# Kernel optimization log

Hardware: AMD Instinct MI355X
Metric: run time of the kernel (lower is better)

The kernel has to match this reference:

```python
import jax, jax.numpy as jnp
import numpy as np

D = 1024      # hidden_size
H = 16        # num_heads
HD = D // H   # head_dim = 64
FF = 4096     # intermediate_size
DEPTH = 2
S = 2048      # packed sequence length
NSEG = 4     # number of image segments
EPS = 1e-6


def setup_inputs() -> dict:
    key = jax.random.key(0)
    ks = jax.random.split(key, 8)
    hidden_states = jax.random.normal(ks[0], (S, D), jnp.float32)
    cu_seqlens = jnp.arange(NSEG + 1, dtype=jnp.int32) * (S // NSEG)
    # rotary embedding like RiceRotaryEmbedding(head_dim//2): freqs of dim HD//4
    # per spatial axis, h/w concatenated -> HD//2, then duplicated -> HD
    inv_freq = 1.0 / (10000.0 ** (jnp.arange(0, HD // 2, 2, dtype=jnp.float32) / (HD // 2)))
    pos = jnp.arange(S, dtype=jnp.float32)
    freqs = jnp.outer(pos, inv_freq)                       # [S, HD//4]
    emb = jnp.concatenate([freqs] * 4, axis=-1)            # [S, HD]
    cos, sin = jnp.cos(emb), jnp.sin(emb)

    def w(k, shape, fan):
        return jax.random.normal(k, shape, jnp.float32) / np.sqrt(fan)

    return {
        "hidden_states": hidden_states,
        "cu_seqlens": cu_seqlens,
        "cos": cos,
        "sin": sin,
        "ln1_g": jnp.ones((DEPTH, D), jnp.float32),
        "ln1_b": jnp.zeros((DEPTH, D), jnp.float32),
        "qkv_w": w(ks[1], (DEPTH, D, 3 * D), D),
        "qkv_b": jnp.zeros((DEPTH, 3 * D), jnp.float32),
        "proj_w": w(ks[2], (DEPTH, D, D), D),
        "proj_b": jnp.zeros((DEPTH, D), jnp.float32),
        "ln2_g": jnp.ones((DEPTH, D), jnp.float32),
        "ln2_b": jnp.zeros((DEPTH, D), jnp.float32),
        "fc1_w": w(ks[3], (DEPTH, D, FF), D),
        "fc1_b": jnp.zeros((DEPTH, FF), jnp.float32),
        "fc2_w": w(ks[4], (DEPTH, FF, D), FF),
        "fc2_b": jnp.zeros((DEPTH, D), jnp.float32),
    }


def _ln(x, g, b):
    m = jnp.mean(x, axis=-1, keepdims=True)
    v = jnp.mean(jnp.square(x - m), axis=-1, keepdims=True)
    return (x - m) / jnp.sqrt(v + EPS) * g + b


def _rotate_half(x):
    x1, x2 = jnp.split(x, 2, axis=-1)
    return jnp.concatenate([-x2, x1], axis=-1)


def reference(hidden_states, cu_seqlens, cos, sin,
              ln1_g, ln1_b, qkv_w, qkv_b, proj_w, proj_b,
              ln2_g, ln2_b, fc1_w, fc1_b, fc2_w, fc2_b):
    S_, D_ = hidden_states.shape
    # segment id per token from cu_seqlens -> block-diagonal additive mask
    seg = jnp.searchsorted(cu_seqlens[1:], jnp.arange(S_, dtype=jnp.int32), side="right")
    neg = jnp.finfo(jnp.float32).min
    bias = jnp.where(seg[:, None] == seg[None, :], 0.0, neg)   # [S, S]
    cos_e = cos[:, None, :]  # broadcast over heads, [S,1,HD]
    sin_e = sin[:, None, :]
    scale = 1.0 / np.sqrt(HD)

    x = hidden_states
    for i in range(DEPTH):
        # --- attention ---
        h = _ln(x, ln1_g[i], ln1_b[i])
        qkv = h @ qkv_w[i] + qkv_b[i]                           # [S, 3D]
        q, k, v = [t.reshape(S_, H, HD) for t in jnp.split(qkv, 3, axis=-1)]
        q = q * cos_e + _rotate_half(q) * sin_e
        k = k * cos_e + _rotate_half(k) * sin_e
        scores = jnp.einsum("shd,thd->hst", q, k) * scale + bias  # [H,S,S]
        w_ = jax.nn.softmax(scores.astype(jnp.float32), axis=-1)
        ao = jnp.einsum("hst,thd->shd", w_, v).reshape(S_, D_)
        x = x + ao @ proj_w[i] + proj_b[i]
        # --- mlp ---
        h2 = _ln(x, ln2_g[i], ln2_b[i])
        x = x + jax.nn.gelu(h2 @ fc1_w[i] + fc1_b[i], approximate=False) @ fc2_w[i] + fc2_b[i]
    return x
```

## Files before the change

### kernel.cpp

```cpp
#include <hip/hip_runtime.h>
#include <hip/hip_bf16.h>
#include <math.h>

#define Dm 1024
#define Hn 16
#define HDm 64
#define FFm 4096
#define Sn 2048
#define SEG 512
#define EPSV 1e-6f

typedef __attribute__((ext_vector_type(4))) float f32x4;
typedef __attribute__((ext_vector_type(8))) short s16x8;
typedef __attribute__((ext_vector_type(4))) short s16x4;

__device__ inline short f2bf(float f) {
  __hip_bfloat16 h = __float2bfloat16(f);
  short s;
  __builtin_memcpy(&s, &h, 2);
  return s;
}
__device__ inline float bf2f(short s) {
  unsigned u = ((unsigned)(unsigned short)s) << 16;
  float f;
  __builtin_memcpy(&f, &u, 4);
  return f;
}

__device__ inline float wred_sum(float v) {
#pragma unroll
  for (int m = 32; m > 0; m >>= 1) v += __shfl_xor(v, m, 64);
  return v;
}

__device__ inline void gld16(const short* g, short* lds_base) {
  __builtin_amdgcn_global_load_lds(
      (const __attribute__((address_space(1))) void*)g,
      (__attribute__((address_space(3))) void*)lds_base, 16, 0, 0);
}

__global__ __launch_bounds__(256) void ln_kernel(const float* __restrict__ x,
                                                 const float* __restrict__ g,
                                                 const float* __restrict__ b,
                                                 short* __restrict__ out) {
  const int row = blockIdx.x;
  const int tid = threadIdx.x;
  f32x4 v = *reinterpret_cast<const f32x4*>(x + (size_t)row * Dm + tid * 4);
  float s1 = v.x + v.y + v.z + v.w;
  float s2 = v.x * v.x + v.y * v.y + v.z * v.z + v.w * v.w;
  s1 = wred_sum(s1);
  s2 = wred_sum(s2);
  __shared__ float t1[4], t2[4];
  if ((tid & 63) == 0) { t1[tid >> 6] = s1; t2[tid >> 6] = s2; }
  __syncthreads();
  s1 = t1[0] + t1[1] + t1[2] + t1[3];
  s2 = t2[0] + t2[1] + t2[2] + t2[3];
  const float mean = s1 * (1.0f / Dm);
  const float var = s2 * (1.0f / Dm) - mean * mean;
  const float rstd = rsqrtf(var + EPSV);
  f32x4 gv = *reinterpret_cast<const f32x4*>(g + tid * 4);
  f32x4 bv = *reinterpret_cast<const f32x4*>(b + tid * 4);
  s16x4 o;
#pragma unroll
  for (int j = 0; j < 4; ++j)
    o[j] = f2bf((v[j] - mean) * rstd * gv[j] + bv[j]);
  *reinterpret_cast<s16x4*>(out + (size_t)row * Dm + tid * 4) = o;
}

template <int SPLIT>
__global__ __launch_bounds__(256) void redln_bf(const short* __restrict__ pb,
                                                const float* __restrict__ bias,
                                                const float* __restrict__ res,
                                                const float* __restrict__ g,
                                                const float* __restrict__ b,
                                                float* __restrict__ xout,
                                                short* __restrict__ h) {
  const int row = blockIdx.x;
  const int tid = threadIdx.x;
  const size_t idx = (size_t)row * Dm + tid * 4;
  f32x4 o = *reinterpret_cast<const f32x4*>(res + idx);
  o += *reinterpret_cast<const f32x4*>(bias + tid * 4);
#pragma unroll
  for (int s = 0; s < SPLIT; ++s) {
    s16x4 v = *reinterpret_cast<const s16x4*>(pb + (size_t)s * Sn * Dm + idx);
#pragma unroll
    for (int j = 0; j < 4; ++j) o[j] += bf2f(v[j]);
  }
  *reinterpret_cast<f32x4*>(xout + idx) = o;
  float s1 = o.x + o.y + o.z + o.w;
  float s2 = o.x * o.x + o.y * o.y + o.z * o.z + o.w * o.w;
  s1 = wred_sum(s1);
  s2 = wred_sum(s2);
  __shared__ float t1[4], t2[4];
  if ((tid & 63) == 0) { t1[tid >> 6] = s1; t2[tid >> 6] = s2; }
  __syncthreads();
  s1 = t1[0] + t1[1] + t1[2] + t1[3];
  s2 = t2[0] + t2[1] + t2[2] + t2[3];
  const float mean = s1 * (1.0f / Dm);
  const float var = s2 * (1.0f / Dm) - mean * mean;
  const float rstd = rsqrtf(var + EPSV);
  f32x4 gv = *reinterpret_cast<const f32x4*>(g + tid * 4);
  f32x4 bv = *reinterpret_cast<const f32x4*>(b + tid * 4);
  s16x4 ho;
#pragma unroll
  for (int j = 0; j < 4; ++j)
    ho[j] = f2bf((o[j] - mean) * rstd * gv[j] + bv[j]);
  *reinterpret_cast<s16x4*>(h + idx) = ho;
}

template <int SPLIT>
__global__ __launch_bounds__(256) void fcred_bf(const short* __restrict__ pb,
                                                const float* __restrict__ bias,
                                                const float* __restrict__ res,
                                                float* __restrict__ out) {
  const size_t i = ((size_t)blockIdx.x * 256 + threadIdx.x) * 4;
  f32x4 o = *reinterpret_cast<const f32x4*>(res + i);
  o += *reinterpret_cast<const f32x4*>(bias + (i & (Dm - 1)));
#pragma unroll
  for (int s = 0; s < SPLIT; ++s) {
    s16x4 v = *reinterpret_cast<const s16x4*>(pb + (size_t)s * Sn * Dm + i);
#pragma unroll
    for (int j = 0; j < 4; ++j) o[j] += bf2f(v[j]);
  }
  *reinterpret_cast<f32x4*>(out + i) = o;
}

__global__ __launch_bounds__(256) void wt_kernel(const float* __restrict__ W,
                                                 short* __restrict__ Wt,
                                                 int K, int N, int ldw) {
  __shared__ float t[32][33];
  const int n0 = blockIdx.x * 32, k0 = blockIdx.y * 32;
  const int tx = threadIdx.x & 31, ty = threadIdx.x >> 5;
#pragma unroll
  for (int r = 0; r < 32; r += 8)
    t[r + ty][tx] = W[(size_t)(k0 + r + ty) * ldw + n0 + tx];
  __syncthreads();
#pragma unroll
  for (int r = 0; r < 32; r += 8)
    Wt[(size_t)(n0 + r + ty) * K + k0 + tx] = f2bf(t[tx][r + ty]);
}

__global__ __launch_bounds__(256) void wtb_kernel(const short* __restrict__ V,
                                                  short* __restrict__ Vt,
                                                  int K, int N, int ldv) {
  __shared__ short t[32][34];
  const int n0 = blockIdx.x * 32, k0 = blockIdx.y * 32;
  const int tx = threadIdx.x & 31, ty = threadIdx.x >> 5;
#pragma unroll
  for (int r = 0; r < 32; r += 8)
    t[r + ty][tx] = V[(size_t)(k0 + r + ty) * ldv + n0 + tx];
  __syncthreads();
#pragma unroll
  for (int r = 0; r < 32; r += 8)
    Vt[(size_t)(n0 + r + ty) * K + k0 + tx] = t[tx][r + ty];
}

__global__ __launch_bounds__(512, 2) void qksoftpv_kernel(const short* __restrict__ qkvb,
                                                          const short* __restrict__ vT,
                                                          short* __restrict__ ao) {
  __shared__ short Qs[128 * 64];
  __shared__ short Ks[512 * 64];
  __shared__ short Vs[64 * 512];
  __shared__ float red[128][4];
  const int tid = threadIdx.x;
  const int lane = tid & 63;
  const int wave = tid >> 6;
  const int wm = wave >> 2, wn = wave & 3;
  const int l15 = lane & 15, lg = lane >> 4, rx = l15 & 7;
  const int qblk = blockIdx.x;
  const int z = blockIdx.y;
  const int seg = z & 3, head = z >> 2;

  const int srow = tid >> 3;
  const int sch = ((tid & 7) ^ (srow & 7)) * 8;

  const short* Qg = qkvb + (size_t)(seg * SEG + qblk * 128 + srow) * 3072 +
                    head * HDm + sch;
  const short* Kg = qkvb + (size_t)(seg * SEG + srow) * 3072 + Dm +
                    head * HDm + sch;
#pragma unroll
  for (int j = 0; j < 2; ++j)
    gld16(Qg + (size_t)(j * 64) * 3072, &Qs[(j * 64 + wave * 8) * 64]);
#pragma unroll
  for (int j = 0; j < 8; ++j)
    gld16(Kg + (size_t)(j * 64) * 3072, &Ks[(j * 64 + wave * 8) * 64]);
  {
    const short* Vg = vT + (size_t)(head * 64) * Sn + seg * SEG;
#pragma unroll
    for (int j = 0; j < 8; ++j) {
      const int d = j * 8 + wave;
      const int c = (lane & ~7) | ((lane & 7) ^ (d & 7));
      gld16(Vg + (size_t)d * Sn + c * 8, &Vs[d * 512]);
    }
  }
  asm volatile("s_waitcnt vmcnt(8)" ::: "memory");
  __builtin_amdgcn_s_barrier();
  __builtin_amdgcn_sched_barrier(0);

  f32x4 acc[4][8] = {};
#pragma unroll
  for (int kc = 0; kc < 8; kc += 4) {
    s16x8 af[4], bf8[8];
#pragma unroll
    for (int f = 0; f < 4; ++f)
      af[f] = *reinterpret_cast<const s16x8*>(
          &Qs[(wm * 64 + f * 16 + l15) * 64 + (((lg + kc) ^ rx) << 3)]);
#pragma unroll
    for (int f = 0; f < 8; ++f)
      bf8[f] = *reinterpret_cast<const s16x8*>(
          &Ks[(wn * 128 + f * 16 + l15) * 64 + (((lg + kc) ^ rx) << 3)]);
#pragma unroll
    for (int fi = 0; fi < 4; ++fi)
#pragma unroll
      for (int fj = 0; fj < 8; ++fj)
        acc[fi][fj] = __builtin_amdgcn_mfma_f32_16x16x32_bf16(
            af[fi], bf8[fj], acc[fi][fj], 0, 0, 0);
  }

  float Ms[4][4];
#pragma unroll
  for (int fi = 0; fi < 4; ++fi) {
#pragma unroll
    for (int r = 0; r < 4; ++r) {
      float m = acc[fi][0][r];
#pragma unroll
      for (int fj = 1; fj < 8; ++fj) m = fmaxf(m, acc[fi][fj][r]);
#pragma unroll
      for (int d = 1; d < 16; d <<= 1) m = fmaxf(m, __shfl_xor(m, d, 64));
      Ms[fi][r] = m;
    }
  }
  if (l15 == 0) {
#pragma unroll
    for (int fi = 0; fi < 4; ++fi)
#pragma unroll
      for (int r = 0; r < 4; ++r)
        red[wm * 64 + fi * 16 + lg * 4 + r][wn] = Ms[fi][r];
  }
  __syncthreads();
#pragma unroll
  for (int fi = 0; fi < 4; ++fi) {
#pragma unroll
    for (int r = 0; r < 4; ++r) {
      const int row = wm * 64 + fi * 16 + lg * 4 + r;
      float m = fmaxf(fmaxf(red[row][0], red[row][1]),
                      fmaxf(red[row][2], red[row][3]));
      Ms[fi][r] = m * 0.125f;
    }
  }
  __syncthreads();

  float Sv[4][4];
#pragma unroll
  for (int fi = 0; fi < 4; ++fi) {
#pragma unroll
    for (int r = 0; r < 4; ++r) {
      float s = 0.f;
#pragma unroll
      for (int fj = 0; fj < 8; ++fj) {
        float pv = __expf(acc[fi][fj][r] * 0.125f - Ms[fi][r]);
        acc[fi][fj][r] = pv;
        s += pv;
      }
#pragma unroll
      for (int d = 1; d < 16; d <<= 1) s += __shfl_xor(s, d, 64);
      Sv[fi][r] = s;
    }
  }
  if (l15 == 0) {
#pragma unroll
    for (int fi = 0; fi < 4; ++fi)
#pragma unroll
      for (int r = 0; r < 4; ++r)
        red[wm * 64 + fi * 16 + lg * 4 + r][wn] = Sv[fi][r];
  }
  __syncthreads();

  asm volatile("s_waitcnt vmcnt(0)" ::: "memory");

  short* Ps = Ks;
  f32x4 pv[4] = {};
  const int q2 = wave * 16 + l15;
  const int sxr = (q2 ^ (q2 >> 3)) & 7;
#pragma unroll
  for (int kh = 0; kh < 2; ++kh) {
    if ((wn >> 1) == kh) {
#pragma unroll
      for (int fi = 0; fi < 4; ++fi)
#pragma unroll
        for (int fj = 0; fj < 8; ++fj)
#pragma unroll
          for (int r = 0; r < 4; ++r) {
            const int q = wm * 64 + fi * 16 + lg * 4 + r;
            const int kp = (wn & 1) * 128 + fj * 16 + l15;
            const int c = kp >> 3;
            const int sxw = (q ^ (q >> 3)) & 7;
            const int cs = (c & 24) | ((c & 7) ^ sxw);
            Ps[q * 256 + cs * 8 + (kp & 7)] = f2bf(acc[fi][fj][r]);
          }
    }
    __syncthreads();
#pragma unroll
    for (int ks = 0; ks < 8; ++ks) {
      const int ca = ks * 4 + lg;
      const int csa = (ca & 24) | ((ca & 7) ^ sxr);
      s16x8 pa = *reinterpret_cast<const s16x8*>(&Ps[q2 * 256 + csa * 8]);
#pragma unroll
      for (int fj = 0; fj < 4; ++fj) {
        const int d = fj * 16 + l15;
        const int cb = kh * 32 + ks * 4 + lg;
        const int csb = (cb & ~7) | ((cb & 7) ^ (d & 7));
        s16x8 pb = *reinterpret_cast<const s16x8*>(&Vs[d * 512 + csb * 8]);
        pv[fj] = __builtin_amdgcn_mfma_f32_16x16x32_bf16(pa, pb, pv[fj], 0, 0, 0);
      }
    }
    __syncthreads();
  }

#pragma unroll
  for (int r = 0; r < 4; ++r) {
    const int q2o = wave * 16 + lg * 4 + r;
    const float inv =
        1.0f / (red[q2o][0] + red[q2o][1] + red[q2o][2] + red[q2o][3]);
    const size_t rowg = (size_t)(seg * SEG + qblk * 128 + q2o) * Dm + head * 64;
#pragma unroll
    for (int fj = 0; fj < 4; ++fj)
      ao[rowg + fj * 16 + l15] = f2bf(pv[fj][r] * inv);
  }
}

struct GemmArgs {
  const short* A; int lda;
  const short* B; int ldb;
  void* C; int ldc;
  int M, N, K;
  const float* bias;
  const float* cosb; const float* sinb;
  float scale;
};

template <int BM, int BN, int SPLIT, int MODE>
__global__ __launch_bounds__(256) void gemm6(GemmArgs p) {
  constexpr int WN = 2;
  constexpr int WM = 2;
  constexpr int FI = BM / WM / 16;
  constexpr int FJ = BN / WN / 16;
  const int z = blockIdx.z;
  const short* A = p.A;
  const short* B = p.B;
  char* Cb = (char*)p.C;
  int kbase = 0, nkt = p.K >> 6;
  const int gx = gridDim.x;
  const int nwg = gx * gridDim.y;
  const int orig = blockIdx.y * gx + blockIdx.x;
  const int sid = (orig & 7) * (nwg >> 3) + (orig >> 3);
  const int tileM = (sid / gx) * BM;
  const int tileN = (sid % gx) * BN;
  if (MODE == 3 || MODE == 6) {
    kbase = z * (p.K / SPLIT);
    nkt = (p.K / SPLIT) >> 6;
    Cb += (size_t)z * p.M * p.N * ((MODE == 3) ? 4 : 2);
  }
  __shared__ short As[BM * 64];
  __shared__ short Bs[BN * 64];
  const int tid = threadIdx.x;
  const int lane = tid & 63;
  const int wave = tid >> 6;
  const int l15 = lane & 15;
  const int lg = lane >> 4;
  const int rx = l15 & 7;
  const int wr = (wave / WN) * (BM / WM);
  const int wc = (wave % WN) * (BN / WN);
  const int srow = lane >> 3;
  const int scol = ((lane & 7) ^ srow) * 8;

  f32x4 acc[FI][FJ] = {};

  const short* Ag = A + (size_t)(tileM + wave * 8 + srow) * p.lda + scol + kbase;
  const short* Bg = B + (size_t)(tileN + wave * 8 + srow) * p.ldb + scol + kbase;

  for (int kt = 0; kt < nkt; ++kt) {
    const int k0 = kt * 64;
#pragma unroll
    for (int j = 0; j < BM / 32; ++j)
      gld16(Ag + (size_t)(j * 32) * p.lda + k0, &As[(j * 32 + wave * 8) * 64]);
#pragma unroll
    for (int j = 0; j < BN / 32; ++j)
      gld16(Bg + (size_t)(j * 32) * p.ldb + k0, &Bs[(j * 32 + wave * 8) * 64]);
    __syncthreads();
#pragma unroll
    for (int kk = 0; kk < 64; kk += 32) {
      const int kkc = kk >> 3;
      s16x8 af[FI], bfr[FJ];
#pragma unroll
      for (int f = 0; f < FI; ++f)
        af[f] = *reinterpret_cast<const s16x8*>(
            &As[(wr + f * 16 + l15) * 64 + (((lg + kkc) ^ rx) << 3)]);
#pragma unroll
      for (int f = 0; f < FJ; ++f)
        bfr[f] = *reinterpret_cast<const s16x8*>(
            &Bs[(wc + f * 16 + l15) * 64 + (((lg + kkc) ^ rx) << 3)]);
#pragma unroll
      for (int fi = 0; fi < FI; ++fi)
#pragma unroll
        for (int fj = 0; fj < FJ; ++fj)
          acc[fi][fj] = __builtin_amdgcn_mfma_f32_16x16x32_bf16(
              af[fi], bfr[fj], acc[fi][fj], 0, 0, 0);
    }
    __syncthreads();
  }

  if (MODE == 4) {
    short* Cs = (short*)Cb;
    const bool isqk = (tileN + wc) < 2048;
#pragma unroll
    for (int fi = 0; fi < FI; ++fi) {
#pragma unroll
      for (int fj = 0; fj < FJ; ++fj) {
#pragma unroll
        for (int r = 0; r < 4; ++r) {
          const int row = tileM + wr + fi * 16 + lg * 4 + r;
          const int col = tileN + wc + fj * 16 + l15;
          float a0 = acc[fi][fj][r] + p.bias[col];
          float vout;
          if (isqk) {
            float a1 = acc[fi][fj ^ 2][r] + p.bias[col ^ 32];
            const int dl = fj * 16 + l15;
            const float c = p.cosb[(size_t)row * HDm + dl];
            const float sn = p.sinb[(size_t)row * HDm + dl];
            vout = (fj < 2) ? (a0 * c - a1 * sn) : (a0 * c + a1 * sn);
          } else {
            vout = a0;
          }
          Cs[(size_t)row * p.ldc + col] = f2bf(vout);
        }
      }
    }
    return;
  }

#pragma unroll
  for (int fi = 0; fi < FI; ++fi) {
#pragma unroll
    for (int fj = 0; fj < FJ; ++fj) {
#pragma unroll
      for (int r = 0; r < 4; ++r) {
        const int row = tileM + wr + fi * 16 + lg * 4 + r;
        const int col = tileN + wc + fj * 16 + l15;
        float v = acc[fi][fj][r] * p.scale;
        if (MODE == 5) {
          v += p.bias[col];
          v = 0.5f * v * (1.0f + erff(v * 0.70710678118654752f));
        }
        if (MODE == 5 || MODE == 6)
          reinterpret_cast<short*>(Cb)[(size_t)row * p.ldc + col] = f2bf(v);
        else
          reinterpret_cast<float*>(Cb)[(size_t)row * p.ldc + col] = v;
      }
    }
  }
}

extern "C" void kernel_launch(void* const* d_in, const int* in_sizes, int n_in,
                              void* d_out, int out_size, void* d_ws, size_t ws_size,
                              hipStream_t stream) {
  const float* x0 = (const float*)d_in[0];
  const float* cosb = (const float*)d_in[2];
  const float* sinb = (const float*)d_in[3];
  const float* ln1_g = (const float*)d_in[4];
  const float* ln1_b = (const float*)d_in[5];
  const float* qkv_w = (const float*)d_in[6];
  const float* qkv_b = (const float*)d_in[7];
  const float* proj_w = (const float*)d_in[8];
  const float* proj_b = (const float*)d_in[9];
  const float* ln2_g = (const float*)d_in[10];
  const float* ln2_b = (const float*)d_in[11];
  const float* fc1_w = (const float*)d_in[12];
  const float* fc1_b = (const float*)d_in[13];
  const float* fc2_w = (const float*)d_in[14];
  const float* fc2_b = (const float*)d_in[15];

  char* ws = (char*)d_ws;
  size_t off = 0;
  auto alloc = [&](size_t bytes) {
    void* p = ws + off;
    off += (bytes + 255) & ~(size_t)255;
    return p;
  };
  short* wqkvT = (short*)alloc((size_t)2 * 3072 * 1024 * 2);
  short* wprojT = (short*)alloc((size_t)2 * 1024 * 1024 * 2);
  short* wfc1T = (short*)alloc((size_t)2 * 4096 * 1024 * 2);
  short* wfc2T = (short*)alloc((size_t)2 * 1024 * 4096 * 2);
  float* xbuf = (float*)alloc((size_t)Sn * Dm * 4);
  short* hbuf = (short*)alloc((size_t)Sn * Dm * 2);
  short* qkvb = (short*)alloc((size_t)Sn * 3 * Dm * 2);
  float* pbuf = (float*)alloc((size_t)4 * Sn * Dm * 4);
  short* pbufS = (short*)pbuf;
  short* ao = (short*)alloc((size_t)Sn * Dm * 2);
  short* ffn = (short*)alloc((size_t)Sn * FFm * 2);
  short* vT = ffn;
  (void)ws_size; (void)in_sizes; (void)n_in; (void)out_size;

  for (int i = 0; i < 2; ++i) {
    wt_kernel<<<dim3(96, 32), 256, 0, stream>>>(
        qkv_w + (size_t)i * Dm * 3072, wqkvT + (size_t)i * 3072 * Dm, Dm, 3072, 3072);
    wt_kernel<<<dim3(32, 32), 256, 0, stream>>>(
        proj_w + (size_t)i * Dm * Dm, wprojT + (size_t)i * Dm * Dm, Dm, Dm, Dm);
    wt_kernel<<<dim3(128, 32), 256, 0, stream>>>(
        fc1_w + (size_t)i * Dm * FFm, wfc1T + (size_t)i * FFm * Dm, Dm, FFm, FFm);
    wt_kernel<<<dim3(32, 128), 256, 0, stream>>>(
        fc2_w + (size_t)i * FFm * Dm, wfc2T + (size_t)i * Dm * FFm, FFm, Dm, Dm);
  }

  ln_kernel<<<dim3(Sn), 256, 0, stream>>>(x0, ln1_g, ln1_b, hbuf);

  for (int i = 0; i < 2; ++i) {
    const float* xin = i ? (const float*)xbuf : x0;

    {
      GemmArgs p = {};
      p.A = hbuf; p.lda = Dm;
      p.B = wqkvT + (size_t)i * 3072 * Dm; p.ldb = Dm;
      p.C = qkvb; p.ldc = 3 * Dm;
      p.M = Sn; p.N = 3 * Dm; p.K = Dm;
      p.bias = qkv_b + i * 3 * Dm; p.cosb = cosb; p.sinb = sinb; p.scale = 1.0f;
      gemm6<64, 128, 1, 4><<<dim3(24, 32, 1), 256, 0, stream>>>(p);
    }

    wtb_kernel<<<dim3(32, 64), 256, 0, stream>>>(qkvb + 2 * Dm, vT, Sn, Dm, 3 * Dm);

    qksoftpv_kernel<<<dim3(4, 64), 512, 0, stream>>>(qkvb, vT, ao);

    {
      GemmArgs p = {};
      p.A = ao; p.lda = Dm;
      p.B = wprojT + (size_t)i * Dm * Dm; p.ldb = Dm;
      p.C = pbufS; p.ldc = Dm;
      p.M = Sn; p.N = Dm; p.K = Dm; p.scale = 1.0f;
      gemm6<64, 64, 2, 6><<<dim3(16, 32, 2), 256, 0, stream>>>(p);
    }
    redln_bf<2><<<dim3(Sn), 256, 0, stream>>>(
        pbufS, proj_b + i * Dm, xin, ln2_g + i * Dm, ln2_b + i * Dm, xbuf, hbuf);

    {
      GemmArgs p = {};
      p.A = hbuf; p.lda = Dm;
      p.B = wfc1T + (size_t)i * FFm * Dm; p.ldb = Dm;
      p.C = ffn; p.ldc = FFm;
      p.M = Sn; p.N = FFm; p.K = Dm;
      p.bias = fc1_b + i * FFm; p.scale = 1.0f;
      gemm6<64, 128, 1, 5><<<dim3(32, 32, 1), 256, 0, stream>>>(p);
    }

    {
      GemmArgs p = {};
      p.A = ffn; p.lda = FFm;
      p.B = wfc2T + (size_t)i * Dm * FFm; p.ldb = FFm;
      p.C = pbufS; p.ldc = Dm;
      p.M = Sn; p.N = Dm; p.K = FFm; p.scale = 1.0f;
      gemm6<64, 128, 4, 6><<<dim3(8, 32, 4), 256, 0, stream>>>(p);
    }
    if (i == 0) {
      redln_bf<4><<<dim3(Sn), 256, 0, stream>>>(
          pbufS, fc2_b, xbuf, ln1_g + Dm, ln1_b + Dm, xbuf, hbuf);
    } else {
      fcred_bf<4><<<dim3(Sn * Dm / 1024), 256, 0, stream>>>(
          pbufS, fc2_b + Dm, xbuf, (float*)d_out);
    }
  }
}
```

Measured before the change: 303.6 us.

## Rewrite attention so each wave owns full rows, reading K/V directly from global

Replaces the 512-thread attention kernel, which staged Q, K and V in shared memory and reduced softmax stats across waves, with a 256-thread kernel where each wave handles 16 query rows over the full 512-key segment. Max and sum reductions now stay within a wave, so cross-wave barriers and the reduction buffer go away. K and V fragments are loaded straight from global memory (relying on cache), and only P is staged in LDS per wave. The grid is reordered so head/segment is the fast dimension and doubles the number of blocks. The trade-off is redundant global/L2 traffic for K and V across blocks and higher register pressure from a 32-tile accumulator.

```diff
diff --git a/kernel.cpp b/kernel.cpp
--- a/kernel.cpp
+++ b/kernel.cpp
@@ -155,178 +155,97 @@
     Vt[(size_t)(n0 + r + ty) * K + k0 + tx] = t[tx][r + ty];
 }
 
-__global__ __launch_bounds__(512, 2) void qksoftpv_kernel(const short* __restrict__ qkvb,
-                                                          const short* __restrict__ vT,
-                                                          short* __restrict__ ao) {
-  __shared__ short Qs[128 * 64];
-  __shared__ short Ks[512 * 64];
-  __shared__ short Vs[64 * 512];
-  __shared__ float red[128][4];
+__global__ __launch_bounds__(256, 2) void attn_kernel(const short* __restrict__ qkvb,
+                                                      const short* __restrict__ vT,
+                                                      short* __restrict__ ao) {
+  __shared__ short Ps[4][16][520];
   const int tid = threadIdx.x;
   const int lane = tid & 63;
   const int wave = tid >> 6;
-  const int wm = wave >> 2, wn = wave & 3;
-  const int l15 = lane & 15, lg = lane >> 4, rx = l15 & 7;
-  const int qblk = blockIdx.x;
-  const int z = blockIdx.y;
+  const int l15 = lane & 15, lg = lane >> 4;
+  const int z = blockIdx.x;
+  const int qblk = blockIdx.y;
   const int seg = z & 3, head = z >> 2;
-
-  const int srow = tid >> 3;
-  const int sch = ((tid & 7) ^ (srow & 7)) * 8;
-
-  const short* Qg = qkvb + (size_t)(seg * SEG + qblk * 128 + srow) * 3072 +
-                    head * HDm + sch;
-  const short* Kg = qkvb + (size_t)(seg * SEG + srow) * 3072 + Dm +
-                    head * HDm + sch;
-#pragma unroll
-  for (int j = 0; j < 2; ++j)
-    gld16(Qg + (size_t)(j * 64) * 3072, &Qs[(j * 64 + wave * 8) * 64]);
-#pragma unroll
-  for (int j = 0; j < 8; ++j)
-    gld16(Kg + (size_t)(j * 64) * 3072, &Ks[(j * 64 + wave * 8) * 64]);
-  {
-    const short* Vg = vT + (size_t)(head * 64) * Sn + seg * SEG;
-#pragma unroll
-    for (int j = 0; j < 8; ++j) {
-      const int d = j * 8 + wave;
-      const int c = (lane & ~7) | ((lane & 7) ^ (d & 7));
-      gld16(Vg + (size_t)d * Sn + c * 8, &Vs[d * 512]);
-    }
-  }
-  asm volatile("s_waitcnt vmcnt(8)" ::: "memory");
-  __builtin_amdgcn_s_barrier();
-  __builtin_amdgcn_sched_barrier(0);
-
-  f32x4 acc[4][8] = {};
-#pragma unroll
-  for (int kc = 0; kc < 8; kc += 4) {
-    s16x8 af[4], bf8[8];
-#pragma unroll
-    for (int f = 0; f < 4; ++f)
-      af[f] = *reinterpret_cast<const s16x8*>(
-          &Qs[(wm * 64 + f * 16 + l15) * 64 + (((lg + kc) ^ rx) << 3)]);
-#pragma unroll
-    for (int f = 0; f < 8; ++f)
-      bf8[f] = *reinterpret_cast<const s16x8*>(
-          &Ks[(wn * 128 + f * 16 + l15) * 64 + (((lg + kc) ^ rx) << 3)]);
-#pragma unroll
-    for (int fi = 0; fi < 4; ++fi)
-#pragma unroll
-      for (int fj = 0; fj < 8; ++fj)
-        acc[fi][fj] = __builtin_amdgcn_mfma_f32_16x16x32_bf16(
-            af[fi], bf8[fj], acc[fi][fj], 0, 0, 0);
-  }
-
-  float Ms[4][4];
-#pragma unroll
-  for (int fi = 0; fi < 4; ++fi) {
-#pragma unroll
-    for (int r = 0; r < 4; ++r) {
-      float m = acc[fi][0][r];
-#pragma unroll
-      for (int fj = 1; fj < 8; ++fj) m = fmaxf(m, acc[fi][fj][r]);
-#pragma unroll
-      for (int d = 1; d < 16; d <<= 1) m = fmaxf(m, __shfl_xor(m, d, 64));
-      Ms[fi][r] = m;
-    }
-  }
-  if (l15 == 0) {
-#pragma unroll
-    for (int fi = 0; fi < 4; ++fi)
-#pragma unroll
-      for (int r = 0; r < 4; ++r)
-        red[wm * 64 + fi * 16 + lg * 4 + r][wn] = Ms[fi][r];
-  }
-  __syncthreads();
-#pragma unroll
-  for (int fi = 0; fi < 4; ++fi) {
-#pragma unroll
-    for (int r = 0; r < 4; ++r) {
-      const int row = wm * 64 + fi * 16 + lg * 4 + r;
-      float m = fmaxf(fmaxf(red[row][0], red[row][1]),
-                      fmaxf(red[row][2], red[row][3]));
-      Ms[fi][r] = m * 0.125f;
-    }
-  }
-  __syncthreads();
-
-  float Sv[4][4];
-#pragma unroll
-  for (int fi = 0; fi < 4; ++fi) {
-#pragma unroll
-    for (int r = 0; r < 4; ++r) {
-      float s = 0.f;
-#pragma unroll
-      for (int fj = 0; fj < 8; ++fj) {
-        float pv = __expf(acc[fi][fj][r] * 0.125f - Ms[fi][r]);
-        acc[fi][fj][r] = pv;
+  const int qrow = seg * SEG + qblk * 64 + wave * 16;
+
+  const short* Qg = qkvb + (size_t)(qrow + l15) * 3072 + head * HDm + lg * 8;
+  s16x8 qf0 = *reinterpret_cast<const s16x8*>(Qg);
+  s16x8 qf1 = *reinterpret_cast<const s16x8*>(Qg + 32);
+
+  f32x4 acc[8][4] = {};
+  const short* Kg = qkvb + (size_t)(seg * SEG + l15) * 3072 + Dm + head * HDm + lg * 8;
+#pragma unroll
+  for (int kt = 0; kt < 8; ++kt) {
+#pragma unroll
+    for (int fj = 0; fj < 4; ++fj) {
+      const short* kp = Kg + (size_t)(kt * 64 + fj * 16) * 3072;
+      s16x8 b0 = *reinterpret_cast<const s16x8*>(kp);
+      s16x8 b1 = *reinterpret_cast<const s16x8*>(kp + 32);
+      acc[kt][fj] = __builtin_amdgcn_mfma_f32_16x16x32_bf16(qf0, b0, acc[kt][fj], 0, 0, 0);
+      acc[kt][fj] = __builtin_amdgcn_mfma_f32_16x16x32_bf16(qf1, b1, acc[kt][fj], 0, 0, 0);
+    }
+  }
+
+  float mx[4], inv[4];
+#pragma unroll
+  for (int r = 0; r < 4; ++r) {
+    float m = acc[0][0][r];
+#pragma unroll
+    for (int kt = 0; kt < 8; ++kt)
+#pragma unroll
+      for (int fj = 0; fj < 4; ++fj) m = fmaxf(m, acc[kt][fj][r]);
+#pragma unroll
+    for (int d = 1; d < 16; d <<= 1) m = fmaxf(m, __shfl_xor(m, d, 64));
+    mx[r] = m * 0.125f;
+  }
+#pragma unroll
+  for (int r = 0; r < 4; ++r) {
+    float s = 0.f;
+#pragma unroll
+    for (int kt = 0; kt < 8; ++kt)
+#pragma unroll
+      for (int fj = 0; fj < 4; ++fj) {
+        float pv = __expf(acc[kt][fj][r] * 0.125f - mx[r]);
+        acc[kt][fj][r] = pv;
         s += pv;
       }
 #pragma unroll
-      for (int d = 1; d < 16; d <<= 1) s += __shfl_xor(s, d, 64);
-      Sv[fi][r] = s;
-    }
-  }
-  if (l15 == 0) {
-#pragma unroll
-    for (int fi = 0; fi < 4; ++fi)
+    for (int d = 1; d < 16; d <<= 1) s += __shfl_xor(s, d, 64);
+    inv[r] = 1.0f / s;
+  }
+
+#pragma unroll
+  for (int kt = 0; kt < 8; ++kt)
+#pragma unroll
+    for (int fj = 0; fj < 4; ++fj)
 #pragma unroll
       for (int r = 0; r < 4; ++r)
-        red[wm * 64 + fi * 16 + lg * 4 + r][wn] = Sv[fi][r];
-  }
-  __syncthreads();
-
-  asm volatile("s_waitcnt vmcnt(0)" ::: "memory");
-
-  short* Ps = Ks;
+        Ps[wave][lg * 4 + r][kt * 64 + fj * 16 + l15] = f2bf(acc[kt][fj][r]);
+  asm volatile("s_waitcnt lgkmcnt(0)" ::: "memory");
+  __builtin_amdgcn_sched_barrier(0);
+
   f32x4 pv[4] = {};
-  const int q2 = wave * 16 + l15;
-  const int sxr = (q2 ^ (q2 >> 3)) & 7;
-#pragma unroll
-  for (int kh = 0; kh < 2; ++kh) {
-    if ((wn >> 1) == kh) {
-#pragma unroll
-      for (int fi = 0; fi < 4; ++fi)
-#pragma unroll
-        for (int fj = 0; fj < 8; ++fj)
-#pragma unroll
-          for (int r = 0; r < 4; ++r) {
-            const int q = wm * 64 + fi * 16 + lg * 4 + r;
-            const int kp = (wn & 1) * 128 + fj * 16 + l15;
-            const int c = kp >> 3;
-            const int sxw = (q ^ (q >> 3)) & 7;
-            const int cs = (c & 24) | ((c & 7) ^ sxw);
-            Ps[q * 256 + cs * 8 + (kp & 7)] = f2bf(acc[fi][fj][r]);
-          }
-    }
-    __syncthreads();
-#pragma unroll
-    for (int ks = 0; ks < 8; ++ks) {
-      const int ca = ks * 4 + lg;
-      const int csa = (ca & 24) | ((ca & 7) ^ sxr);
-      s16x8 pa = *reinterpret_cast<const s16x8*>(&Ps[q2 * 256 + csa * 8]);
+  const short* Vg = vT + (size_t)(head * HDm) * Sn + seg * SEG;
+#pragma unroll
+  for (int kt = 0; kt < 8; ++kt)
+#pragma unroll
+    for (int c = 0; c < 2; ++c) {
+      s16x8 pa = *reinterpret_cast<const s16x8*>(
+          &Ps[wave][l15][kt * 64 + c * 32 + lg * 8]);
 #pragma unroll
       for (int fj = 0; fj < 4; ++fj) {
-        const int d = fj * 16 + l15;
-        const int cb = kh * 32 + ks * 4 + lg;
-        const int csb = (cb & ~7) | ((cb & 7) ^ (d & 7));
-        s16x8 pb = *reinterpret_cast<const s16x8*>(&Vs[d * 512 + csb * 8]);
+        s16x8 pb = *reinterpret_cast<const s16x8*>(
+            Vg + (size_t)(fj * 16 + l15) * Sn + kt * 64 + c * 32 + lg * 8);
         pv[fj] = __builtin_amdgcn_mfma_f32_16x16x32_bf16(pa, pb, pv[fj], 0, 0, 0);
       }
     }
-    __syncthreads();
-  }
-
-#pragma unroll
-  for (int r = 0; r < 4; ++r) {
-    const int q2o = wave * 16 + lg * 4 + r;
-    const float inv =
-        1.0f / (red[q2o][0] + red[q2o][1] + red[q2o][2] + red[q2o][3]);
-    const size_t rowg = (size_t)(seg * SEG + qblk * 128 + q2o) * Dm + head * 64;
-#pragma unroll
-    for (int fj = 0; fj < 4; ++fj)
-      ao[rowg + fj * 16 + l15] = f2bf(pv[fj][r] * inv);
-  }
+
+#pragma unroll
+  for (int fj = 0; fj < 4; ++fj)
+#pragma unroll
+    for (int r = 0; r < 4; ++r)
+      ao[(size_t)(qrow + lg * 4 + r) * Dm + head * HDm + fj * 16 + l15] =
+          f2bf(pv[fj][r] * inv[r]);
 }
 
 struct GemmArgs {
@@ -529,7 +448,7 @@
 
     wtb_kernel<<<dim3(32, 64), 256, 0, stream>>>(qkvb + 2 * Dm, vT, Sn, Dm, 3 * Dm);
 
-    qksoftpv_kernel<<<dim3(4, 64), 512, 0, stream>>>(qkvb, vT, ao);
+    attn_kernel<<<dim3(64, 8), 256, 0, stream>>>(qkvb, vT, ao);
 
     {
       GemmArgs p = {};
```

Result: slower. 326.1 us (+7.4%).
